# Optimization experiments

Hardware: AMD Instinct MI355X
Metric: run time of the kernel (lower is better)

## Reference

```python
import jax, jax.numpy as jnp
import numpy as np

N = 50000      # nodes
E = 1_600_000  # edges
D = 512        # input_dim == embedding_dim (see notes: fc_emb output is dead code)
H = 256        # hidden_channels
G = 16         # graphs in the batch


def setup_inputs() -> dict:
    key = jax.random.key(0)
    ks = jax.random.split(key, 16)
    x = jax.random.normal(ks[0], (N, D), dtype=jnp.float32)
    edge_index = jax.random.randint(ks[1], (2, E), 0, N, dtype=jnp.int64)
    batch = jnp.sort(jax.random.randint(ks[2], (N,), 0, G, dtype=jnp.int64))

    def lin(k, fi, fo):
        s = 1.0 / np.sqrt(fi)
        return jax.random.uniform(k, (fi, fo), jnp.float32, -s, s)

    return {
        "x": x,
        "edge_index": edge_index,
        "batch": batch,
        "W1": lin(ks[3], D, H), "b1": jnp.zeros((H,), jnp.float32),
        "W2": lin(ks[4], H, H), "b2": jnp.zeros((H,), jnp.float32),
        "W3": lin(ks[5], H, H), "b3": jnp.zeros((H,), jnp.float32),
        "Wf": lin(ks[6], H, 64), "bf": jnp.zeros((64,), jnp.float32),
        "Wp": lin(ks[7], 64, 1), "bp": jnp.zeros((1,), jnp.float32),
    }


def _gcn_conv(h, src, dst, norm, W, b):
    # GCNConv: out[i] = sum_{j->i} norm_ji * (h[j] @ W) + b  (self-loops included in src/dst)
    m = h @ W                                    # [N, out]  transform first (smaller gather)
    agg = jax.ops.segment_sum(m[src] * norm[:, None], dst, num_segments=N)
    return agg + b


def reference(x, edge_index, batch, W1, b1, W2, b2, W3, b3, Wf, bf, Wp, bp):
    loops = jnp.arange(N, dtype=edge_index.dtype)
    src = jnp.concatenate([edge_index[0], loops])   # [E+N]
    dst = jnp.concatenate([edge_index[1], loops])
    # symmetric normalization D^{-1/2} (A+I) D^{-1/2}; degree over targets incl. self-loops
    deg = jax.ops.segment_sum(jnp.ones_like(dst, jnp.float32), dst, num_segments=N)
    dinv = jnp.where(deg > 0, jax.lax.rsqrt(deg), 0.0)
    norm = dinv[src] * dinv[dst]                    # [E+N]

    h = jax.nn.relu(_gcn_conv(x, src, dst, norm, W1, b1))
    h = jax.nn.relu(_gcn_conv(h, src, dst, norm, W2, b2))
    h = _gcn_conv(h, src, dst, norm, W3, b3)

    # global_mean_pool over graph ids
    counts = jax.ops.segment_sum(jnp.ones((N,), jnp.float32), batch, num_segments=G)
    pooled = jax.ops.segment_sum(h, batch, num_segments=G) / jnp.maximum(counts, 1.0)[:, None]

    # dropout treated as identity (eval-mode determinism for baseline)
    out = pooled @ Wf + bf
    out = out @ Wp + bp
    return jax.nn.sigmoid(out)
```

## Files before the change

### kernel.cpp

```cpp
#include <hip/hip_runtime.h>
#include <hip/hip_bf16.h>

#define NN 50000
#define EE 1600000
#define DD 512
#define HH 256
#define GG 16
#define BK 96
#define NCH 256
#define CHSZ 6250
#define PCH 64

typedef long fp8x8;
typedef __attribute__((ext_vector_type(4))) float f32x4;
typedef __attribute__((ext_vector_type(2))) float f32x2;

__device__ __forceinline__ unsigned char f2fp8(float f) {
    return (unsigned char)(__builtin_amdgcn_cvt_pk_fp8_f32(f, f, 0, false) & 0xff);
}
__device__ __forceinline__ unsigned int pk4fp8(float a, float b, float c, float d) {
    unsigned int r = __builtin_amdgcn_cvt_pk_fp8_f32(a, b, 0, false);
    return __builtin_amdgcn_cvt_pk_fp8_f32(c, d, r, true);
}

__global__ __launch_bounds__(256) void k_hist_cvt(const int* __restrict__ ei,
                                                  unsigned int* __restrict__ histg,
                                                  const float* __restrict__ x, unsigned char* __restrict__ xb,
                                                  const float* __restrict__ W1, const float* __restrict__ W2,
                                                  const float* __restrict__ W3, unsigned char* __restrict__ W1t,
                                                  unsigned char* __restrict__ W2t, unsigned char* __restrict__ W3t) {
    __shared__ unsigned int hp[6250];
    int b = blockIdx.x, t = threadIdx.x;
    if (b < 512) {
        int j = b >> 1, half = b & 1;
        int dlo = half * 25000;
        for (int i = t; i < 6250; i += 256) hp[i] = 0;
        __syncthreads();
        int base = j * CHSZ;
        for (int k = 0; k < 25; ++k) {
            int o = k * 256 + t;
            if (o < CHSZ) {
                int d = ei[EE + base + o];
                unsigned int ld = (unsigned)(d - dlo);
                if (ld < 25000u) atomicAdd(&hp[ld >> 2], 1u << ((ld & 3) * 8));
            }
        }
        __syncthreads();
        unsigned int* dst = histg + (size_t)j * 12500 + half * 6250;
        for (int i = t; i < 6250; i += 256) dst[i] = hp[i];
    } else if (b < 6762) {
        size_t i0 = ((size_t)(b - 512) * 256 + t) * 16;
        float4 v0 = *(const float4*)(x + i0);
        float4 v1 = *(const float4*)(x + i0 + 4);
        float4 v2 = *(const float4*)(x + i0 + 8);
        float4 v3 = *(const float4*)(x + i0 + 12);
        uint4 o;
        o.x = pk4fp8(v0.x, v0.y, v0.z, v0.w);
        o.y = pk4fp8(v1.x, v1.y, v1.z, v1.w);
        o.z = pk4fp8(v2.x, v2.y, v2.z, v2.w);
        o.w = pk4fp8(v3.x, v3.y, v3.z, v3.w);
        *(uint4*)(xb + i0) = o;
    } else {
        int u = (b - 6762) * 256 + t;
        if (u < 131072) {
            int k = u >> 8, n = u & 255;
            W1t[(size_t)n * 512 + k] = f2fp8(W1[u]);
        } else if (u < 196608) {
            int q = u - 131072; int k = q >> 8, n = q & 255;
            W2t[(size_t)n * 256 + k] = f2fp8(W2[q]);
        } else {
            int q = u - 196608; int k = q >> 8, n = q & 255;
            W3t[(size_t)n * 256 + k] = f2fp8(W3[q]);
        }
    }
}

__global__ __launch_bounds__(256) void k_scan(const unsigned int* __restrict__ histg,
                                              unsigned int* __restrict__ offg,
                                              int* __restrict__ cnt, float* __restrict__ dinv) {
    __shared__ unsigned int part[512];
    int t = threadIdx.x, b = blockIdx.x;
    const int il = t & 31, g = t >> 5;
    const int g4 = b * 32 + il;
    const bool ok = (g4 < 12500);
    unsigned hv[32];
    unsigned s02 = 0, s13 = 0;
    if (ok) {
        const unsigned* hp = histg + (size_t)(g * 32) * 12500 + g4;
        #pragma unroll
        for (int jj = 0; jj < 32; ++jj) hv[jj] = hp[(size_t)jj * 12500];
        #pragma unroll
        for (int jj = 0; jj < 32; ++jj) { s02 += hv[jj] & 0x00ff00ffu; s13 += (hv[jj] >> 8) & 0x00ff00ffu; }
    }
    part[t * 2] = s02; part[t * 2 + 1] = s13;
    __syncthreads();
    unsigned b02 = 0, b13 = 0;
    #pragma unroll
    for (int g2 = 0; g2 < 7; ++g2)
        if (g2 < g) { b02 += part[(g2 * 32 + il) * 2]; b13 += part[(g2 * 32 + il) * 2 + 1]; }
    if (ok && g == 7) {
        unsigned t02 = b02 + s02, t13 = b13 + s13;
        int4 cv; cv.x = (int)(t02 & 0xffffu); cv.y = (int)(t13 & 0xffffu);
        cv.z = (int)(t02 >> 16);      cv.w = (int)(t13 >> 16);
        *(int4*)(cnt + 4 * g4) = cv;
        float4 dv;
        dv.x = rsqrtf((float)cv.x + 1.0f); dv.y = rsqrtf((float)cv.y + 1.0f);
        dv.z = rsqrtf((float)cv.z + 1.0f); dv.w = rsqrtf((float)cv.w + 1.0f);
        *(float4*)(dinv + 4 * g4) = dv;
    }
    if (ok) {
        unsigned r0 = b02 & 0xffffu, r2 = b02 >> 16, r1 = b13 & 0xffffu, r3 = b13 >> 16;
        #pragma unroll
        for (int jj = 0; jj < 32; ++jj) {
            uint2 wv; wv.x = r0 | (r1 << 16); wv.y = r2 | (r3 << 16);
            *(uint2*)(offg + (size_t)(g * 32 + jj) * 25000 + 2 * g4) = wv;
            unsigned h = hv[jj];
            r0 += h & 0xffu; r1 += (h >> 8) & 0xffu; r2 += (h >> 16) & 0xffu; r3 += h >> 24;
        }
    }
}

__global__ __launch_bounds__(256) void k_place(const int* __restrict__ ei,
                                               const unsigned int* __restrict__ offg,
                                               unsigned short* __restrict__ bucket) {
    __shared__ unsigned int cur[3125];
    int b = blockIdx.x, t = threadIdx.x;
    int x8 = b & 7, j = b >> 3;
    int lo = x8 * CHSZ;
    for (int i = t; i < 3125; i += 256) cur[i] = 0;
    __syncthreads();
    int base = j * CHSZ;
    for (int k = 0; k < 25; ++k) {
        int o = k * 256 + t;
        if (o < CHSZ) {
            int d = ei[EE + base + o];
            unsigned ld = (unsigned)(d - lo);
            if (ld < 6250u) {
                int s = ei[base + o];
                unsigned old = atomicAdd(&cur[ld >> 1], (ld & 1) ? 65536u : 1u);
                unsigned rank = (ld & 1) ? (old >> 16) : (old & 0xffffu);
                unsigned ov = offg[j * 25000 + (d >> 1)];
                unsigned pos = ((d & 1) ? (ov >> 16) : (ov & 0xffffu)) + rank;
                if (pos < BK) bucket[(size_t)d * BK + pos] = (unsigned short)s;
            }
        }
    }
}

__global__ __launch_bounds__(256) void k_gemm_fp8(const unsigned char* __restrict__ A,
                                                  const unsigned char* __restrict__ Bt,
                                                  const float* __restrict__ dinv,
                                                  unsigned char* __restrict__ C, int M, int K) {
    __shared__ unsigned char As[2][8192];
    __shared__ unsigned char Bs[2][8192];
    const int tid  = threadIdx.x;
    const int wave = tid >> 6;
    const int lane = tid & 63;
    const int row0 = blockIdx.x * 128;
    const int col0 = blockIdx.y * 128;
    const int wr = wave & 1;
    const int wc = wave >> 1;
    const int l15 = lane & 15;
    const int quad = lane >> 4;

    const int srow = (wave << 4) + (lane >> 2);
    const int gk16 = (((lane & 3) ^ (srow & 3)) << 4);
    int arow1 = row0 + srow;      if (arow1 >= M) arow1 = M - 1;
    int arow2 = row0 + srow + 64; if (arow2 >= M) arow2 = M - 1;
    const int brow1 = col0 + srow;
    const int brow2 = brow1 + 64;

#define STAGE(BUF, KB) do {                                                              \
    const unsigned char* ga1_ = A  + (size_t)arow1 * K + (KB) + gk16;                    \
    const unsigned char* ga2_ = A  + (size_t)arow2 * K + (KB) + gk16;                    \
    const unsigned char* gb1_ = Bt + (size_t)brow1 * K + (KB) + gk16;                    \
    const unsigned char* gb2_ = Bt + (size_t)brow2 * K + (KB) + gk16;                    \
    __builtin_amdgcn_global_load_lds((const __attribute__((address_space(1))) void*)ga1_,\
        (__attribute__((address_space(3))) void*)&As[BUF][wave * 1024], 16, 0, 0);       \
    __builtin_amdgcn_global_load_lds((const __attribute__((address_space(1))) void*)ga2_,\
        (__attribute__((address_space(3))) void*)&As[BUF][4096 + wave * 1024], 16, 0, 0);\
    __builtin_amdgcn_global_load_lds((const __attribute__((address_space(1))) void*)gb1_,\
        (__attribute__((address_space(3))) void*)&Bs[BUF][wave * 1024], 16, 0, 0);       \
    __builtin_amdgcn_global_load_lds((const __attribute__((address_space(1))) void*)gb2_,\
        (__attribute__((address_space(3))) void*)&Bs[BUF][4096 + wave * 1024], 16, 0, 0);\
} while (0)

    f32x4 acc[4][4];
    #pragma unroll
    for (int i = 0; i < 4; ++i)
        #pragma unroll
        for (int j = 0; j < 4; ++j)
            acc[i][j] = (f32x4){0.f, 0.f, 0.f, 0.f};

    const int NT = K >> 6;
    STAGE(0, 0);
    __syncthreads();

    for (int t = 0; t < NT; ++t) {
        const int cb = t & 1;
        if (t + 1 < NT) STAGE(cb ^ 1, (t + 1) << 6);

        fp8x8 af[2][4], bfr[2][4];
        #pragma unroll
        for (int kk = 0; kk < 2; ++kk) {
            const int csw = (((kk * 2 + (quad >> 1)) ^ (l15 & 3)) << 4) + ((quad & 1) << 3);
            #pragma unroll
            for (int mi = 0; mi < 4; ++mi) {
                af[kk][mi]  = *(const fp8x8*)&As[cb][(wr * 64 + mi * 16 + l15) * 64 + csw];
                bfr[kk][mi] = *(const fp8x8*)&Bs[cb][(wc * 64 + mi * 16 + l15) * 64 + csw];
            }
        }
        #pragma unroll
        for (int kk = 0; kk < 2; ++kk)
            #pragma unroll
            for (int mi = 0; mi < 4; ++mi)
                #pragma unroll
                for (int ni = 0; ni < 4; ++ni)
                    acc[mi][ni] = __builtin_amdgcn_mfma_f32_16x16x32_fp8_fp8(af[kk][mi], bfr[kk][ni], acc[mi][ni], 0, 0, 0);

        __syncthreads();
    }
#undef STAGE

    #pragma unroll
    for (int mi = 0; mi < 4; ++mi) {
        #pragma unroll
        for (int r = 0; r < 4; ++r) {
            int grow = row0 + wr * 64 + mi * 16 + quad * 4 + r;
            if (grow < M) {
                float ds = dinv[grow];
                #pragma unroll
                for (int ni = 0; ni < 4; ++ni) {
                    int gcol = col0 + wc * 64 + ni * 16 + l15;
                    C[(size_t)grow * 256 + gcol] = f2fp8(ds * acc[mi][ni][r]);
                }
            }
        }
    }
}

__global__ __launch_bounds__(256) void k_agg(const unsigned int* __restrict__ m,
                                             const float* __restrict__ bias,
                                             const float* __restrict__ dinv, const int* __restrict__ cnt,
                                             const unsigned short* __restrict__ bucket,
                                             unsigned int* __restrict__ outb,
                                             int do_relu) {
    int lane = threadIdx.x & 63;
    int node = blockIdx.x * 4 + (threadIdx.x >> 6);
    if (node >= NN) return;
    const unsigned int* mrow = m + lane;
    unsigned int v = mrow[(size_t)node * 64];
    f32x2 lo = __builtin_amdgcn_cvt_pk_f32_fp8(v, false);
    f32x2 hi = __builtin_amdgcn_cvt_pk_f32_fp8(v, true);
    float4 acc = make_float4(lo.x, lo.y, hi.x, hi.y);
    int n = cnt[node]; if (n > BK) n = BK;
    const unsigned short* cs = bucket + (size_t)node * BK;
    int p = 0;
    for (; p + 16 <= n; p += 16) {
        uint4 iv0 = *(const uint4*)(cs + p);
        uint4 iv1 = *(const uint4*)(cs + p + 8);
        unsigned int u0 = mrow[(size_t)(iv0.x & 0xffffu) * 64];
        unsigned int u1 = mrow[(size_t)(iv0.x >> 16)    * 64];
        unsigned int u2 = mrow[(size_t)(iv0.y & 0xffffu) * 64];
        unsigned int u3 = mrow[(size_t)(iv0.y >> 16)    * 64];
        unsigned int u4 = mrow[(size_t)(iv0.z & 0xffffu) * 64];
        unsigned int u5 = mrow[(size_t)(iv0.z >> 16)    * 64];
        unsigned int u6 = mrow[(size_t)(iv0.w & 0xffffu) * 64];
        unsigned int u7 = mrow[(size_t)(iv0.w >> 16)    * 64];
        unsigned int u8 = mrow[(size_t)(iv1.x & 0xffffu) * 64];
        unsigned int u9 = mrow[(size_t)(iv1.x >> 16)    * 64];
        unsigned int ua = mrow[(size_t)(iv1.y & 0xffffu) * 64];
        unsigned int ub = mrow[(size_t)(iv1.y >> 16)    * 64];
        unsigned int uc = mrow[(size_t)(iv1.z & 0xffffu) * 64];
        unsigned int ud = mrow[(size_t)(iv1.z >> 16)    * 64];
        unsigned int ue = mrow[(size_t)(iv1.w & 0xffffu) * 64];
        unsigned int uf = mrow[(size_t)(iv1.w >> 16)    * 64];
        f32x2 a0 = __builtin_amdgcn_cvt_pk_f32_fp8(u0, false), b0 = __builtin_amdgcn_cvt_pk_f32_fp8(u0, true);
        f32x2 a1 = __builtin_amdgcn_cvt_pk_f32_fp8(u1, false), b1 = __builtin_amdgcn_cvt_pk_f32_fp8(u1, true);
        f32x2 a2 = __builtin_amdgcn_cvt_pk_f32_fp8(u2, false), b2 = __builtin_amdgcn_cvt_pk_f32_fp8(u2, true);
        f32x2 a3 = __builtin_amdgcn_cvt_pk_f32_fp8(u3, false), b3 = __builtin_amdgcn_cvt_pk_f32_fp8(u3, true);
        f32x2 a4 = __builtin_amdgcn_cvt_pk_f32_fp8(u4, false), b4 = __builtin_amdgcn_cvt_pk_f32_fp8(u4, true);
        f32x2 a5 = __builtin_amdgcn_cvt_pk_f32_fp8(u5, false), b5 = __builtin_amdgcn_cvt_pk_f32_fp8(u5, true);
        f32x2 a6 = __builtin_amdgcn_cvt_pk_f32_fp8(u6, false), b6 = __builtin_amdgcn_cvt_pk_f32_fp8(u6, true);
        f32x2 a7 = __builtin_amdgcn_cvt_pk_f32_fp8(u7, false), b7 = __builtin_amdgcn_cvt_pk_f32_fp8(u7, true);
        f32x2 a8 = __builtin_amdgcn_cvt_pk_f32_fp8(u8, false), b8 = __builtin_amdgcn_cvt_pk_f32_fp8(u8, true);
        f32x2 a9 = __builtin_amdgcn_cvt_pk_f32_fp8(u9, false), b9 = __builtin_amdgcn_cvt_pk_f32_fp8(u9, true);
        f32x2 aa = __builtin_amdgcn_cvt_pk_f32_fp8(ua, false), ba = __builtin_amdgcn_cvt_pk_f32_fp8(ua, true);
        f32x2 ab = __builtin_amdgcn_cvt_pk_f32_fp8(ub, false), bb2 = __builtin_amdgcn_cvt_pk_f32_fp8(ub, true);
        f32x2 ac = __builtin_amdgcn_cvt_pk_f32_fp8(uc, false), bc = __builtin_amdgcn_cvt_pk_f32_fp8(uc, true);
        f32x2 ad = __builtin_amdgcn_cvt_pk_f32_fp8(ud, false), bd = __builtin_amdgcn_cvt_pk_f32_fp8(ud, true);
        f32x2 ae = __builtin_amdgcn_cvt_pk_f32_fp8(ue, false), be = __builtin_amdgcn_cvt_pk_f32_fp8(ue, true);
        f32x2 af2 = __builtin_amdgcn_cvt_pk_f32_fp8(uf, false), bf2 = __builtin_amdgcn_cvt_pk_f32_fp8(uf, true);
        acc.x += (((a0.x + a1.x) + (a2.x + a3.x)) + ((a4.x + a5.x) + (a6.x + a7.x)))
               + (((a8.x + a9.x) + (aa.x + ab.x)) + ((ac.x + ad.x) + (ae.x + af2.x)));
        acc.y += (((a0.y + a1.y) + (a2.y + a3.y)) + ((a4.y + a5.y) + (a6.y + a7.y)))
               + (((a8.y + a9.y) + (aa.y + ab.y)) + ((ac.y + ad.y) + (ae.y + af2.y)));
        acc.z += (((b0.x + b1.x) + (b2.x + b3.x)) + ((b4.x + b5.x) + (b6.x + b7.x)))
               + (((b8.x + b9.x) + (ba.x + bb2.x)) + ((bc.x + bd.x) + (be.x + bf2.x)));
        acc.w += (((b0.y + b1.y) + (b2.y + b3.y)) + ((b4.y + b5.y) + (b6.y + b7.y)))
               + (((b8.y + b9.y) + (ba.y + bb2.y)) + ((bc.y + bd.y) + (be.y + bf2.y)));
    }
    for (; p + 8 <= n; p += 8) {
        uint4 iv0 = *(const uint4*)(cs + p);
        unsigned int u0 = mrow[(size_t)(iv0.x & 0xffffu) * 64];
        unsigned int u1 = mrow[(size_t)(iv0.x >> 16)    * 64];
        unsigned int u2 = mrow[(size_t)(iv0.y & 0xffffu) * 64];
        unsigned int u3 = mrow[(size_t)(iv0.y >> 16)    * 64];
        unsigned int u4 = mrow[(size_t)(iv0.z & 0xffffu) * 64];
        unsigned int u5 = mrow[(size_t)(iv0.z >> 16)    * 64];
        unsigned int u6 = mrow[(size_t)(iv0.w & 0xffffu) * 64];
        unsigned int u7 = mrow[(size_t)(iv0.w >> 16)    * 64];
        f32x2 a0 = __builtin_amdgcn_cvt_pk_f32_fp8(u0, false), b0 = __builtin_amdgcn_cvt_pk_f32_fp8(u0, true);
        f32x2 a1 = __builtin_amdgcn_cvt_pk_f32_fp8(u1, false), b1 = __builtin_amdgcn_cvt_pk_f32_fp8(u1, true);
        f32x2 a2 = __builtin_amdgcn_cvt_pk_f32_fp8(u2, false), b2 = __builtin_amdgcn_cvt_pk_f32_fp8(u2, true);
        f32x2 a3 = __builtin_amdgcn_cvt_pk_f32_fp8(u3, false), b3 = __builtin_amdgcn_cvt_pk_f32_fp8(u3, true);
        f32x2 a4 = __builtin_amdgcn_cvt_pk_f32_fp8(u4, false), b4 = __builtin_amdgcn_cvt_pk_f32_fp8(u4, true);
        f32x2 a5 = __builtin_amdgcn_cvt_pk_f32_fp8(u5, false), b5 = __builtin_amdgcn_cvt_pk_f32_fp8(u5, true);
        f32x2 a6 = __builtin_amdgcn_cvt_pk_f32_fp8(u6, false), b6 = __builtin_amdgcn_cvt_pk_f32_fp8(u6, true);
        f32x2 a7 = __builtin_amdgcn_cvt_pk_f32_fp8(u7, false), b7 = __builtin_amdgcn_cvt_pk_f32_fp8(u7, true);
        acc.x += ((a0.x + a1.x) + (a2.x + a3.x)) + ((a4.x + a5.x) + (a6.x + a7.x));
        acc.y += ((a0.y + a1.y) + (a2.y + a3.y)) + ((a4.y + a5.y) + (a6.y + a7.y));
        acc.z += ((b0.x + b1.x) + (b2.x + b3.x)) + ((b4.x + b5.x) + (b6.x + b7.x));
        acc.w += ((b0.y + b1.y) + (b2.y + b3.y)) + ((b4.y + b5.y) + (b6.y + b7.y));
    }
    for (; p < n; ++p) {
        int s = cs[p];
        unsigned int u = mrow[(size_t)s * 64];
        f32x2 a = __builtin_amdgcn_cvt_pk_f32_fp8(u, false);
        f32x2 b = __builtin_amdgcn_cvt_pk_f32_fp8(u, true);
        acc.x += a.x; acc.y += a.y; acc.z += b.x; acc.w += b.y;
    }
    float di = dinv[node];
    const float4 bb = *(const float4*)(bias + lane * 4);
    acc.x = acc.x * di + bb.x; acc.y = acc.y * di + bb.y;
    acc.z = acc.z * di + bb.z; acc.w = acc.w * di + bb.w;
    if (do_relu) {
        acc.x = fmaxf(acc.x, 0.f); acc.y = fmaxf(acc.y, 0.f);
        acc.z = fmaxf(acc.z, 0.f); acc.w = fmaxf(acc.w, 0.f);
    }
    outb[(size_t)node * 64 + lane] = pk4fp8(acc.x, acc.y, acc.z, acc.w);
}

__global__ __launch_bounds__(256) void k_poolA(const unsigned int* __restrict__ h,
                                               const int* __restrict__ batch,
                                               float* __restrict__ partial) {
    __shared__ float red[1024];
    __shared__ int bnd[2];
    int g = blockIdx.x >> 6, c = blockIdx.x & (PCH - 1);
    int t = threadIdx.x, sub = t >> 6, fd = t & 63;
    if (t < 2) {
        int key = g + t;
        int lo = 0, hi = NN;
        while (lo < hi) { int mid = (lo + hi) >> 1; if (batch[mid] < key) lo = mid + 1; else hi = mid; }
        bnd[t] = lo;
    }
    __syncthreads();
    int start = bnd[0], len = bnd[1] - bnd[0];
    int r0 = start + (int)(((long long)len * c) >> 6);
    int r1 = start + (int)(((long long)len * (c + 1)) >> 6);
    float a0 = 0.f, a1 = 0.f, a2 = 0.f, a3 = 0.f;
    for (int i = r0 + sub; i < r1; i += 4) {
        unsigned int u = h[(size_t)i * 64 + fd];
        f32x2 lo = __builtin_amdgcn_cvt_pk_f32_fp8(u, false);
        f32x2 hi = __builtin_amdgcn_cvt_pk_f32_fp8(u, true);
        a0 += lo.x; a1 += lo.y; a2 += hi.x; a3 += hi.y;
    }
    red[sub * 256 + fd * 4 + 0] = a0;
    red[sub * 256 + fd * 4 + 1] = a1;
    red[sub * 256 + fd * 4 + 2] = a2;
    red[sub * 256 + fd * 4 + 3] = a3;
    __syncthreads();
    if (t < 64) {
        float4 s;
        s.x = (red[t * 4 + 0] + red[256 + t * 4 + 0]) + (red[512 + t * 4 + 0] + red[768 + t * 4 + 0]);
        s.y = (red[t * 4 + 1] + red[256 + t * 4 + 1]) + (red[512 + t * 4 + 1] + red[768 + t * 4 + 1]);
        s.z = (red[t * 4 + 2] + red[256 + t * 4 + 2]) + (red[512 + t * 4 + 2] + red[768 + t * 4 + 2]);
        s.w = (red[t * 4 + 3] + red[256 + t * 4 + 3]) + (red[512 + t * 4 + 3] + red[768 + t * 4 + 3]);
        *(float4*)(partial + (size_t)c * (GG * 256) + g * 256 + t * 4) = s;
    }
}

__global__ __launch_bounds__(256) void k_poolB(const float* __restrict__ partial,
                                               const int* __restrict__ batch,
                                               const float* __restrict__ Wf, const float* __restrict__ bf,
                                               const float* __restrict__ Wp, const float* __restrict__ bp,
                                               float* __restrict__ out) {
    __shared__ float pg[256];
    __shared__ float zred[4][64];
    __shared__ float zs[64];
    __shared__ int bnd[2];
    int g = blockIdx.x, t = threadIdx.x;
    if (t < 2) {
        int key = g + t;
        int lo = 0, hi = NN;
        while (lo < hi) { int mid = (lo + hi) >> 1; if (batch[mid] < key) lo = mid + 1; else hi = mid; }
        bnd[t] = lo;
    }
    float s = 0.f;
    #pragma unroll 8
    for (int c = 0; c < PCH; ++c) s += partial[(size_t)c * (GG * 256) + g * 256 + t];
    pg[t] = s;
    __syncthreads();
    float inv = 1.f / fmaxf((float)(bnd[1] - bnd[0]), 1.f);
    int j = t & 63, part = t >> 6;
    float zp = 0.f;
    for (int k = part * 64; k < part * 64 + 64; ++k) zp += pg[k] * Wf[k * 64 + j];
    zred[part][j] = zp;
    __syncthreads();
    if (t < 64) {
        float z = ((zred[0][t] + zred[1][t]) + (zred[2][t] + zred[3][t])) * inv + bf[t];
        zs[t] = z * Wp[t];
    }
    __syncthreads();
    if (t == 0) {
        float o = 0.f;
        for (int j2 = 0; j2 < 64; ++j2) o += zs[j2];
        o += bp[0];
        out[g] = 1.f / (1.f + expf(-o));
    }
}

extern "C" void kernel_launch(void* const* d_in, const int* in_sizes, int n_in,
                              void* d_out, int out_size, void* d_ws, size_t ws_size,
                              hipStream_t stream) {
    const float* x   = (const float*)d_in[0];
    const int*   ei  = (const int*)d_in[1];
    const int*   bat = (const int*)d_in[2];
    const float* W1  = (const float*)d_in[3];
    const float* b1  = (const float*)d_in[4];
    const float* W2  = (const float*)d_in[5];
    const float* b2  = (const float*)d_in[6];
    const float* W3  = (const float*)d_in[7];
    const float* b3  = (const float*)d_in[8];
    const float* Wf  = (const float*)d_in[9];
    const float* bf  = (const float*)d_in[10];
    const float* Wp  = (const float*)d_in[11];
    const float* bp  = (const float*)d_in[12];
    float* out = (float*)d_out;

    char* w = (char*)d_ws;
    unsigned char* xb  = (unsigned char*)w;  w += (size_t)NN * DD;
    unsigned char* mb  = (unsigned char*)w;  w += (size_t)NN * HH;
    unsigned char* hb  = (unsigned char*)w;  w += (size_t)NCH * 25000 * 4;
    unsigned char* hb2 = (unsigned char*)w;  w += (size_t)NCH * 25000 * 4;
    unsigned char* W1t = (unsigned char*)w;  w += (size_t)DD * HH;
    unsigned char* W2t = (unsigned char*)w;  w += (size_t)HH * HH;
    unsigned char* W3t = (unsigned char*)w;  w += (size_t)HH * HH;
    float* dinv   = (float*)w;               w += (size_t)NN * 4;
    int*   cnt    = (int*)w;                 w += (size_t)NN * 4;
    unsigned short* bucket = (unsigned short*)w; w += (size_t)NN * BK * 2;
    float* partial = (float*)w;              w += (size_t)PCH * GG * HH * 4;

    unsigned int* histg = (unsigned int*)hb;
    unsigned int* offg  = (unsigned int*)hb2;

    k_hist_cvt<<<7786, 256, 0, stream>>>(ei, histg, x, xb, W1, W2, W3, W1t, W2t, W3t);
    k_scan<<<391, 256, 0, stream>>>(histg, offg, cnt, dinv);
    k_place<<<2048, 256, 0, stream>>>(ei, offg, bucket);

    dim3 gg((NN + 127) / 128, 2);
    k_gemm_fp8<<<gg, 256, 0, stream>>>(xb, W1t, dinv, mb, NN, DD);
    k_agg<<<(NN + 3) / 4, 256, 0, stream>>>((const unsigned int*)mb, b1, dinv, cnt, bucket,
                                            (unsigned int*)hb, 1);
    k_gemm_fp8<<<gg, 256, 0, stream>>>(hb, W2t, dinv, mb, NN, HH);
    k_agg<<<(NN + 3) / 4, 256, 0, stream>>>((const unsigned int*)mb, b2, dinv, cnt, bucket,
                                            (unsigned int*)hb2, 1);
    k_gemm_fp8<<<gg, 256, 0, stream>>>(hb2, W3t, dinv, mb, NN, HH);
    k_agg<<<(NN + 3) / 4, 256, 0, stream>>>((const unsigned int*)mb, b3, dinv, cnt, bucket,
                                            (unsigned int*)hb, 0);

    k_poolA<<<GG * PCH, 256, 0, stream>>>((const unsigned int*)hb, bat, partial);
    k_poolB<<<GG, 256, 0, stream>>>(partial, bat, Wf, bf, Wp, bp, out);
}
```

Baseline: 492.2 us.

## Widen GEMM tile to full 256 columns and merge place kernel over node range

The FP8 GEMM now computes a 128x256 output tile per block, so each block covers all output columns and the A tile is read once instead of twice. This doubles the accumulators and B LDS per block, which raises register and LDS pressure and may lower occupancy. The edge placement kernel drops the 8-way split of the destination range. Each block now handles one edge chunk over all nodes with a 12500-word LDS counter array holding 8-bit packed per-node ranks. This cuts redundant edge reads but relies on per-chunk per-node counts staying below 256.

Result: slower. 527.5 us (+7.2%).

```diff
diff --git a/kernel.cpp b/kernel.cpp
--- a/kernel.cpp
+++ b/kernel.cpp
@@ -123,26 +123,21 @@
 __global__ __launch_bounds__(256) void k_place(const int* __restrict__ ei,
                                                const unsigned int* __restrict__ offg,
                                                unsigned short* __restrict__ bucket) {
-    __shared__ unsigned int cur[3125];
+    __shared__ unsigned int cur[12500];
     int b = blockIdx.x, t = threadIdx.x;
-    int x8 = b & 7, j = b >> 3;
-    int lo = x8 * CHSZ;
-    for (int i = t; i < 3125; i += 256) cur[i] = 0;
-    __syncthreads();
-    int base = j * CHSZ;
+    for (int i = t; i < 12500; i += 256) cur[i] = 0;
+    __syncthreads();
+    int base = b * CHSZ;
     for (int k = 0; k < 25; ++k) {
         int o = k * 256 + t;
         if (o < CHSZ) {
             int d = ei[EE + base + o];
-            unsigned ld = (unsigned)(d - lo);
-            if (ld < 6250u) {
-                int s = ei[base + o];
-                unsigned old = atomicAdd(&cur[ld >> 1], (ld & 1) ? 65536u : 1u);
-                unsigned rank = (ld & 1) ? (old >> 16) : (old & 0xffffu);
-                unsigned ov = offg[j * 25000 + (d >> 1)];
-                unsigned pos = ((d & 1) ? (ov >> 16) : (ov & 0xffffu)) + rank;
-                if (pos < BK) bucket[(size_t)d * BK + pos] = (unsigned short)s;
-            }
+            int s = ei[base + o];
+            unsigned old = atomicAdd(&cur[d >> 2], 1u << ((d & 3) * 8));
+            unsigned rank = (old >> ((d & 3) * 8)) & 0xffu;
+            unsigned ov = offg[(size_t)b * 25000 + (d >> 1)];
+            unsigned pos = ((d & 1) ? (ov >> 16) : (ov & 0xffffu)) + rank;
+            if (pos < BK) bucket[(size_t)d * BK + pos] = (unsigned short)s;
         }
     }
 }
@@ -152,12 +147,11 @@
                                                   const float* __restrict__ dinv,
                                                   unsigned char* __restrict__ C, int M, int K) {
     __shared__ unsigned char As[2][8192];
-    __shared__ unsigned char Bs[2][8192];
+    __shared__ unsigned char Bs[2][16384];
     const int tid  = threadIdx.x;
     const int wave = tid >> 6;
     const int lane = tid & 63;
     const int row0 = blockIdx.x * 128;
-    const int col0 = blockIdx.y * 128;
     const int wr = wave & 1;
     const int wc = wave >> 1;
     const int l15 = lane & 15;
@@ -167,29 +161,24 @@
     const int gk16 = (((lane & 3) ^ (srow & 3)) << 4);
     int arow1 = row0 + srow;      if (arow1 >= M) arow1 = M - 1;
     int arow2 = row0 + srow + 64; if (arow2 >= M) arow2 = M - 1;
-    const int brow1 = col0 + srow;
-    const int brow2 = brow1 + 64;
-
+
+#define GLOAD(SRC, DST) __builtin_amdgcn_global_load_lds(                                \
+        (const __attribute__((address_space(1))) void*)(SRC),                            \
+        (__attribute__((address_space(3))) void*)(DST), 16, 0, 0)
 #define STAGE(BUF, KB) do {                                                              \
-    const unsigned char* ga1_ = A  + (size_t)arow1 * K + (KB) + gk16;                    \
-    const unsigned char* ga2_ = A  + (size_t)arow2 * K + (KB) + gk16;                    \
-    const unsigned char* gb1_ = Bt + (size_t)brow1 * K + (KB) + gk16;                    \
-    const unsigned char* gb2_ = Bt + (size_t)brow2 * K + (KB) + gk16;                    \
-    __builtin_amdgcn_global_load_lds((const __attribute__((address_space(1))) void*)ga1_,\
-        (__attribute__((address_space(3))) void*)&As[BUF][wave * 1024], 16, 0, 0);       \
-    __builtin_amdgcn_global_load_lds((const __attribute__((address_space(1))) void*)ga2_,\
-        (__attribute__((address_space(3))) void*)&As[BUF][4096 + wave * 1024], 16, 0, 0);\
-    __builtin_amdgcn_global_load_lds((const __attribute__((address_space(1))) void*)gb1_,\
-        (__attribute__((address_space(3))) void*)&Bs[BUF][wave * 1024], 16, 0, 0);       \
-    __builtin_amdgcn_global_load_lds((const __attribute__((address_space(1))) void*)gb2_,\
-        (__attribute__((address_space(3))) void*)&Bs[BUF][4096 + wave * 1024], 16, 0, 0);\
+    GLOAD(A  + (size_t)arow1 * K + (KB) + gk16,        &As[BUF][wave * 1024]);           \
+    GLOAD(A  + (size_t)arow2 * K + (KB) + gk16,        &As[BUF][4096 + wave * 1024]);    \
+    GLOAD(Bt + (size_t)(srow)       * K + (KB) + gk16, &Bs[BUF][wave * 1024]);           \
+    GLOAD(Bt + (size_t)(srow +  64) * K + (KB) + gk16, &Bs[BUF][4096  + wave * 1024]);   \
+    GLOAD(Bt + (size_t)(srow + 128) * K + (KB) + gk16, &Bs[BUF][8192  + wave * 1024]);   \
+    GLOAD(Bt + (size_t)(srow + 192) * K + (KB) + gk16, &Bs[BUF][12288 + wave * 1024]);   \
 } while (0)
 
-    f32x4 acc[4][4];
+    f32x4 acc[4][8];
     #pragma unroll
     for (int i = 0; i < 4; ++i)
         #pragma unroll
-        for (int j = 0; j < 4; ++j)
+        for (int j = 0; j < 8; ++j)
             acc[i][j] = (f32x4){0.f, 0.f, 0.f, 0.f};
 
     const int NT = K >> 6;
@@ -200,27 +189,29 @@
         const int cb = t & 1;
         if (t + 1 < NT) STAGE(cb ^ 1, (t + 1) << 6);
 
-        fp8x8 af[2][4], bfr[2][4];
+        fp8x8 af[2][4], bfr[2][8];
         #pragma unroll
         for (int kk = 0; kk < 2; ++kk) {
             const int csw = (((kk * 2 + (quad >> 1)) ^ (l15 & 3)) << 4) + ((quad & 1) << 3);
             #pragma unroll
-            for (int mi = 0; mi < 4; ++mi) {
+            for (int mi = 0; mi < 4; ++mi)
                 af[kk][mi]  = *(const fp8x8*)&As[cb][(wr * 64 + mi * 16 + l15) * 64 + csw];
-                bfr[kk][mi] = *(const fp8x8*)&Bs[cb][(wc * 64 + mi * 16 + l15) * 64 + csw];
-            }
+            #pragma unroll
+            for (int ni = 0; ni < 8; ++ni)
+                bfr[kk][ni] = *(const fp8x8*)&Bs[cb][(wc * 128 + ni * 16 + l15) * 64 + csw];
         }
         #pragma unroll
         for (int kk = 0; kk < 2; ++kk)
             #pragma unroll
             for (int mi = 0; mi < 4; ++mi)
                 #pragma unroll
-                for (int ni = 0; ni < 4; ++ni)
+                for (int ni = 0; ni < 8; ++ni)
                     acc[mi][ni] = __builtin_amdgcn_mfma_f32_16x16x32_fp8_fp8(af[kk][mi], bfr[kk][ni], acc[mi][ni], 0, 0, 0);
 
         __syncthreads();
     }
 #undef STAGE
+#undef GLOAD
 
     #pragma unroll
     for (int mi = 0; mi < 4; ++mi) {
@@ -230,8 +221,8 @@
             if (grow < M) {
                 float ds = dinv[grow];
                 #pragma unroll
-                for (int ni = 0; ni < 4; ++ni) {
-                    int gcol = col0 + wc * 64 + ni * 16 + l15;
+                for (int ni = 0; ni < 8; ++ni) {
+                    int gcol = wc * 128 + ni * 16 + l15;
                     C[(size_t)grow * 256 + gcol] = f2fp8(ds * acc[mi][ni][r]);
                 }
             }
@@ -456,9 +447,9 @@
 
     k_hist_cvt<<<7786, 256, 0, stream>>>(ei, histg, x, xb, W1, W2, W3, W1t, W2t, W3t);
     k_scan<<<391, 256, 0, stream>>>(histg, offg, cnt, dinv);
-    k_place<<<2048, 256, 0, stream>>>(ei, offg, bucket);
-
-    dim3 gg((NN + 127) / 128, 2);
+    k_place<<<NCH, 256, 0, stream>>>(ei, offg, bucket);
+
+    dim3 gg((NN + 127) / 128);
     k_gemm_fp8<<<gg, 256, 0, stream>>>(xb, W1t, dinv, mb, NN, DD);
     k_agg<<<(NN + 3) / 4, 256, 0, stream>>>((const unsigned int*)mb, b1, dinv, cnt, bucket,
                                             (unsigned int*)hb, 1);
```
